# Kernel optimization log

Hardware: AMD Instinct MI355X
Metric: run time of the kernel (lower is better)

Reference implementation:

```python
import jax, jax.numpy as jnp
import numpy as np

NUM_POINTS = 33  # must be 2n+1
N_T = 4_194_304  # number of time samples


def setup_inputs() -> dict:
    key = jax.random.key(0)
    k1, k2 = jax.random.split(key)
    x = jax.random.uniform(k1, (N_T,), dtype=jnp.float32)  # t in [0,1]
    P = jax.random.uniform(k2, (NUM_POINTS, 5), dtype=jnp.float32)
    P = (P - P.mean()) / P.std()  # mimics initLayers normalization
    return {"x": x, "P": P}


def _basis(d):
    """d: (N,1) -> quadratic Bezier basis (N,3) = [1, d, d^2] @ B."""
    B = jnp.array([[1., 0., 0.], [-2., 2., 0.], [1., -2., 1.]], dtype=d.dtype)
    tpow = jnp.concatenate([jnp.ones_like(d), d, d * d], axis=1)  # (N,3)
    return tpow @ B


def _forward(x, P):
    num_points = P.shape[0]
    S = num_points - 2  # num_splines
    p = P[:, :2]   # (num_points, 2) means
    s = P[:, 2:]   # (num_points, 3) packed symmetric 2x2: [a, b, c] -> [[a,b],[b,c]]
    # new_sigma_mat = sigma_mat^T @ sigma_mat (sigma_mat symmetric) packed back to 3 entries
    a, b, c = s[:, 0], s[:, 1], s[:, 2]
    sig = jnp.stack([a * a + b * b, b * (a + c), b * b + c * c], axis=1)  # (num_points, 3)

    t = x[:, None]                       # (N,1)
    N = x.shape[0]
    mu0 = jnp.zeros((N, 2), x.dtype)
    sg0 = jnp.zeros((N, 3), x.dtype)
    Pn0 = p[:3]                          # (3,2)
    Sn0 = sig[:3]                        # (3,3)
    ivals = jnp.arange(S - 1, dtype=x.dtype)
    Sm1 = jnp.asarray(S - 1, x.dtype)

    def step(carry, xs):
        Pn, Sn, mu, sg = carry
        i, p_next, s_next = xs
        d = (t * Sm1 - i) * 0.5                      # (N,1)
        choice = ((d >= 0) & (d <= 0.5)).astype(x.dtype)
        cw = jnp.cos(jnp.pi * d) ** 2
        sw = jnp.sin(jnp.pi * d) ** 2
        # mean control-point recurrence
        p0 = (Pn[0] + Pn[2]) / 4 + Pn[1] / 2
        p2 = p_next
        p1 = 2.0 * (Pn[2] - (p0 + p2) / 4)
        Pn2 = jnp.stack([p0, p1, p2])                # (3,2)
        f_prev = _basis(d + 0.5) @ Pn                # (N,2)
        f_curr = _basis(d) @ Pn2
        mu = (1 - choice) * mu + choice * (cw * f_prev + sw * f_curr)
        # variance control-point recurrence
        s0 = (Sn[0] + Sn[2]) / 16 + Sn[1] / 4
        s2 = s_next
        s1 = 4.0 * (Sn[2] - (s0 + s2) / 16)
        Sn2 = jnp.stack([s0, s1, s2])                # (3,3)
        g_prev = (_basis(d + 0.5) ** 2) @ Sn         # (N,3)
        g_curr = (_basis(d) ** 2) @ Sn2
        sg = (1 - choice) * sg + choice * (cw ** 2 * g_prev + sw ** 2 * g_curr)
        return (Pn2, Sn2, mu, sg), None

    (_, _, mu, sg), _ = jax.lax.scan(step, (Pn0, Sn0, mu0, sg0), (ivals, p[3:], sig[3:]))
    return mu, sg


def reference(x, P):
    return _forward(x, P)
```

## Files before the change

kernel.cpp:

```cpp
#include <hip/hip_runtime.h>
#include <math.h>

#define NENT 33
#define NREC 30
#define RECF 12
#define PPT 4
#define NBLK 2048

__global__ __launch_bounds__(256) void yuksel_fused(
    const float* __restrict__ x, const float* __restrict__ P,
    float* __restrict__ out, int N)
{
    __shared__ __align__(16) float qtab[5][NREC][RECF];
    __shared__ float stage[5][NENT];
    const int tid = threadIdx.x;

    if (tid < NENT) {
        const int e = tid;
        float vals[5];
        if (e == 1) {
            float r0[5], r1[5], r2[5];
            for (int r = 0; r < 3; ++r) {
                float* dst = r==0 ? r0 : (r==1 ? r1 : r2);
                float a = P[r*5+2], b = P[r*5+3], c = P[r*5+4];
                dst[0] = P[r*5+0]; dst[1] = P[r*5+1];
                dst[2] = a*a + b*b; dst[3] = b*(a+c); dst[4] = b*b + c*c;
            }
            for (int k = 0; k < 2; ++k) vals[k] = (r0[k]+r2[k])*0.25f   + r1[k]*0.5f;
            for (int k = 2; k < 5; ++k) vals[k] = (r0[k]+r2[k])*0.0625f + r1[k]*0.25f;
        } else {
            float a = P[e*5+2], b = P[e*5+3], c = P[e*5+4];
            vals[0] = P[e*5+0]; vals[1] = P[e*5+1];
            vals[2] = a*a + b*b; vals[3] = b*(a+c); vals[4] = b*b + c*c;
        }
#pragma unroll
        for (int k = 0; k < 5; ++k) stage[k][e] = vals[k];
    }
    __syncthreads();

    if (tid < 5*NREC) {
        const int r = tid / 5, k = tid % 5;
        float4 v = make_float4(stage[k][r], stage[k][r+1], stage[k][r+2], stage[k][r+3]);
        *reinterpret_cast<float4*>(&qtab[k][r][0]) = v;
    }
    __syncthreads();

    const long long stride = (long long)gridDim.x * 256 * PPT;
    for (long long j0 = ((long long)blockIdx.x * 256 + tid) * PPT; j0 < N; j0 += stride) {
        float4 xv = *reinterpret_cast<const float4*>(x + j0);
        float xs[PPT] = { xv.x, xv.y, xv.z, xv.w };
        float mu[2*PPT], sg[3*PPT];

#pragma unroll
        for (int q = 0; q < PPT; ++q) {
            float u  = xs[q] * 30.0f;
            float fi = fminf(fmaxf(floorf(u), 0.0f), 29.0f);
            int   i  = (int)fi;
            float d  = (u - fi) * 0.5f;
            float e  = d + 0.5f;

            float omd = 1.0f - d, ome = 1.0f - e;
            float bc0 = omd*omd, bc1 = 2.0f*d*omd, bc2 = d*d;
            float bp0 = ome*ome, bp1 = 2.0f*e*ome, bp2 = e*e;

            float cw  = 0.5f + 0.5f*__builtin_amdgcn_cosf(d);
            float sw  = 1.0f - cw;
            float cw2 = cw*cw, sw2 = sw*sw;

            float w0 = cw*(bp0 - 0.5f*bp1);
            float w1 = 2.0f*cw*bp1 + sw*(bc0 - 0.5f*bc1);
            float w2 = cw*(bp2 - 0.5f*bp1) + 2.0f*sw*bc1;
            float w3 = sw*(bc2 - 0.5f*bc1);
            float a0 = bp0*bp0, a1 = bp1*bp1, a2 = bp2*bp2;
            float c0 = bc0*bc0, c1 = bc1*bc1, c2 = bc2*bc2;
            float v0 = cw2*(a0 - 0.25f*a1);
            float v1 = 4.0f*cw2*a1 + sw2*(c0 - 0.25f*c1);
            float v2 = cw2*(a2 - 0.25f*a1) + 4.0f*sw2*c1;
            float v3 = sw2*(c2 - 0.25f*c1);

            float4 px = *reinterpret_cast<const float4*>(&qtab[0][i][0]);
            float4 py = *reinterpret_cast<const float4*>(&qtab[1][i][0]);
            float4 s0 = *reinterpret_cast<const float4*>(&qtab[2][i][0]);
            float4 s1 = *reinterpret_cast<const float4*>(&qtab[3][i][0]);
            float4 s2 = *reinterpret_cast<const float4*>(&qtab[4][i][0]);

            mu[2*q+0] = w0*px.x + w1*px.y + w2*px.z + w3*px.w;
            mu[2*q+1] = w0*py.x + w1*py.y + w2*py.z + w3*py.w;
            sg[3*q+0] = v0*s0.x + v1*s0.y + v2*s0.z + v3*s0.w;
            sg[3*q+1] = v0*s1.x + v1*s1.y + v2*s1.z + v3*s1.w;
            sg[3*q+2] = v0*s2.x + v1*s2.y + v2*s2.z + v3*s2.w;
        }

        float4* muOut = reinterpret_cast<float4*>(out + 2*j0);
        muOut[0] = make_float4(mu[0], mu[1], mu[2], mu[3]);
        muOut[1] = make_float4(mu[4], mu[5], mu[6], mu[7]);
        float4* sgOut = reinterpret_cast<float4*>(out + (size_t)2*N + 3*j0);
        sgOut[0] = make_float4(sg[0], sg[1], sg[2],  sg[3]);
        sgOut[1] = make_float4(sg[4], sg[5], sg[6],  sg[7]);
        sgOut[2] = make_float4(sg[8], sg[9], sg[10], sg[11]);
    }
}

extern "C" void kernel_launch(void* const* d_in, const int* in_sizes, int n_in,
                              void* d_out, int out_size, void* d_ws, size_t ws_size,
                              hipStream_t stream) {
    const float* x = (const float*)d_in[0];
    const float* P = (const float*)d_in[1];
    float* out = (float*)d_out;
    int N = in_sizes[0];

    const int threads = 256;
    const int per_block = threads * PPT;
    long long ntiles = (N + per_block - 1) / per_block;
    int blocks = (int)(ntiles < NBLK ? ntiles : NBLK);
    yuksel_fused<<<blocks, threads, 0, stream>>>(x, P, out, N);
}
```

Baseline: 27.17 us.

## Store control-point table as packed bf16 and simplify basis weight algebra

Packs the per-segment control-point table in shared memory as bf16 pairs in uint2 words instead of float4, halving LDS read width per lookup. It also rewrites the blending-weight polynomials in factored closed form to cut ALU work. The kernel is likely bound by memory bandwidth, given 4M points and 20 bytes of output each. The bf16 table reduces the precision of control points and may break tolerance.

```diff
diff --git a/kernel.cpp b/kernel.cpp
--- a/kernel.cpp
+++ b/kernel.cpp
@@ -2,17 +2,24 @@
 #include <math.h>
 
 #define NENT 33
-#define NREC 30
-#define RECF 12
-#define PPT 4
+#define NQ   30
+#define PPT  4
 #define NBLK 2048
+
+__device__ __forceinline__ unsigned short f2bf(float f) {
+    unsigned int b = __float_as_uint(f);
+    unsigned int r = (b + 0x7FFFu + ((b >> 16) & 1u)) >> 16;
+    return (unsigned short)r;
+}
+__device__ __forceinline__ float bflo(unsigned int w) { return __uint_as_float(w << 16); }
+__device__ __forceinline__ float bfhi(unsigned int w) { return __uint_as_float(w & 0xFFFF0000u); }
 
 __global__ __launch_bounds__(256) void yuksel_fused(
     const float* __restrict__ x, const float* __restrict__ P,
     float* __restrict__ out, int N)
 {
-    __shared__ __align__(16) float qtab[5][NREC][RECF];
     __shared__ float stage[5][NENT];
+    __shared__ uint2 qtab[5][NQ];
     const int tid = threadIdx.x;
 
     if (tid < NENT) {
@@ -38,10 +45,11 @@
     }
     __syncthreads();
 
-    if (tid < 5*NREC) {
-        const int r = tid / 5, k = tid % 5;
-        float4 v = make_float4(stage[k][r], stage[k][r+1], stage[k][r+2], stage[k][r+3]);
-        *reinterpret_cast<float4*>(&qtab[k][r][0]) = v;
+    if (tid < 5*NQ) {
+        const int k = tid / NQ, e = tid % NQ;
+        unsigned int h0 = f2bf(stage[k][e+0]), h1 = f2bf(stage[k][e+1]);
+        unsigned int h2 = f2bf(stage[k][e+2]), h3 = f2bf(stage[k][e+3]);
+        qtab[k][e] = make_uint2(h0 | (h1 << 16), h2 | (h3 << 16));
     }
     __syncthreads();
 
@@ -57,38 +65,37 @@
             float fi = fminf(fmaxf(floorf(u), 0.0f), 29.0f);
             int   i  = (int)fi;
             float d  = (u - fi) * 0.5f;
-            float e  = d + 0.5f;
-
-            float omd = 1.0f - d, ome = 1.0f - e;
-            float bc0 = omd*omd, bc1 = 2.0f*d*omd, bc2 = d*d;
-            float bp0 = ome*ome, bp1 = 2.0f*e*ome, bp2 = e*e;
 
             float cw  = 0.5f + 0.5f*__builtin_amdgcn_cosf(d);
             float sw  = 1.0f - cw;
             float cw2 = cw*cw, sw2 = sw*sw;
 
-            float w0 = cw*(bp0 - 0.5f*bp1);
-            float w1 = 2.0f*cw*bp1 + sw*(bc0 - 0.5f*bc1);
-            float w2 = cw*(bp2 - 0.5f*bp1) + 2.0f*sw*bc1;
-            float w3 = sw*(bc2 - 0.5f*bc1);
-            float a0 = bp0*bp0, a1 = bp1*bp1, a2 = bp2*bp2;
-            float c0 = bc0*bc0, c1 = bc1*bc1, c2 = bc2*bc2;
-            float v0 = cw2*(a0 - 0.25f*a1);
-            float v1 = 4.0f*cw2*a1 + sw2*(c0 - 0.25f*c1);
-            float v2 = cw2*(a2 - 0.25f*a1) + 4.0f*sw2*c1;
-            float v3 = sw2*(c2 - 0.25f*c1);
+            float omd  = 1.0f - d;
+            float om2d = 1.0f - 2.0f*d;
+            float g    = d * om2d;
+            float w0 = -cw * g;
+            float w3 = -sw * g;
+            float w1 = cw*(1.0f - 4.0f*d*d) + sw*omd*om2d;
+            float w2 = cw*d*(1.0f + 2.0f*d) + 4.0f*sw*d*omd;
 
-            float4 px = *reinterpret_cast<const float4*>(&qtab[0][i][0]);
-            float4 py = *reinterpret_cast<const float4*>(&qtab[1][i][0]);
-            float4 s0 = *reinterpret_cast<const float4*>(&qtab[2][i][0]);
-            float4 s1 = *reinterpret_cast<const float4*>(&qtab[3][i][0]);
-            float4 s2 = *reinterpret_cast<const float4*>(&qtab[4][i][0]);
+            float hp = 0.5f + d;
+            float q14 = 1.0f - 4.0f*d*d;
+            float v0 = -cw2 * g * (0.5f - d);
+            float v3 = -sw2 * g * d;
+            float v1 = cw2*q14*q14 + sw2*omd*omd*om2d;
+            float v2 = cw2*2.0f*d*hp*hp + 16.0f*sw2*d*d*omd*omd;
 
-            mu[2*q+0] = w0*px.x + w1*px.y + w2*px.z + w3*px.w;
-            mu[2*q+1] = w0*py.x + w1*py.y + w2*py.z + w3*py.w;
-            sg[3*q+0] = v0*s0.x + v1*s0.y + v2*s0.z + v3*s0.w;
-            sg[3*q+1] = v0*s1.x + v1*s1.y + v2*s1.z + v3*s1.w;
-            sg[3*q+2] = v0*s2.x + v1*s2.y + v2*s2.z + v3*s2.w;
+            uint2 rpx = qtab[0][i];
+            uint2 rpy = qtab[1][i];
+            uint2 rs0 = qtab[2][i];
+            uint2 rs1 = qtab[3][i];
+            uint2 rs2 = qtab[4][i];
+
+            mu[2*q+0] = w0*bflo(rpx.x) + w1*bfhi(rpx.x) + w2*bflo(rpx.y) + w3*bfhi(rpx.y);
+            mu[2*q+1] = w0*bflo(rpy.x) + w1*bfhi(rpy.x) + w2*bflo(rpy.y) + w3*bfhi(rpy.y);
+            sg[3*q+0] = v0*bflo(rs0.x) + v1*bfhi(rs0.x) + v2*bflo(rs0.y) + v3*bfhi(rs0.y);
+            sg[3*q+1] = v0*bflo(rs1.x) + v1*bfhi(rs1.x) + v2*bflo(rs1.y) + v3*bfhi(rs1.y);
+            sg[3*q+2] = v0*bflo(rs2.x) + v1*bfhi(rs2.x) + v2*bflo(rs2.y) + v3*bfhi(rs2.y);
         }
 
         float4* muOut = reinterpret_cast<float4*>(out + 2*j0);
```

Result: faster. 26.38 us (-2.9%).
